# Performance work log

Measured on AMD Instinct MI355X. Metric: run time of the kernel, lower is better.

The kernel has to match this reference:

```python
import jax, jax.numpy as jnp
import numpy as np

LN_EPS = 1e-12
CHEB_K = 3
HIDDEN = 64


def _layernorm(x, w, b):
    m = jnp.mean(x, axis=-1, keepdims=True)
    v = jnp.mean((x - m) ** 2, axis=-1, keepdims=True)
    return (x - m) / jnp.sqrt(v + LN_EPS) * w + b


def _magcn(x, node_emb, time_emb, ln_w, ln_b, W_pool, b_pool):
    # x: [B,N,C]; node_emb: [N,D]; W_pool: [D,K,C,O]; b_pool: [D,O]
    e = _layernorm(node_emb + time_emb[None, :], ln_w, ln_b)  # dropout = identity (eval)
    supports = jax.nn.softmax(e @ e.T, axis=1)                # [N,N]
    N = e.shape[0]
    Ts = [jnp.eye(N, dtype=x.dtype), supports]
    for _ in range(2, CHEB_K):
        Ts.append(2.0 * supports @ Ts[-1] - Ts[-2])
    S = jnp.stack(Ts, axis=0)                                 # [K,N,N]
    weights = jnp.einsum('nd,dkio->nkio', e, W_pool)          # [N,K,C,O]
    bias = e @ b_pool                                         # [N,O]
    x_g = jnp.einsum('knm,bmc->bnkc', S, x)                   # [B,N,K,C]
    return jnp.einsum('bnki,nkio->bno', x_g, weights) + bias  # [B,N,O]


def setup_inputs() -> dict:
    key = jax.random.key(0)
    ks = jax.random.split(key, 10)
    B, N, C, H, D = 64, 1024, 64, HIDDEN, 16
    return {
        'x': jax.random.normal(ks[0], (B, N, C), jnp.float32),
        'norm_dis_matrix': jax.random.uniform(ks[1], (N, N), jnp.float32),
        'state': jax.random.normal(ks[2], (B, N, H), jnp.float32),
        'node_embeddings': jax.random.normal(ks[3], (N, D), jnp.float32),
        'node_flows': jax.random.normal(ks[4], (B, N), jnp.float32),
        'time_embeddings': jax.random.normal(ks[5], (D,), jnp.float32),
        'gate_W': jax.random.normal(ks[6], (D, CHEB_K, C + H, 2 * H), jnp.float32) * 0.1,
        'gate_b': jax.random.normal(ks[7], (D, 2 * H), jnp.float32) * 0.1,
        'gate_ln_w': jnp.ones((D,), jnp.float32),
        'gate_ln_b': jnp.zeros((D,), jnp.float32),
        'update_W': jax.random.normal(ks[8], (D, CHEB_K, C + H, H), jnp.float32) * 0.1,
        'update_b': jax.random.normal(ks[9], (D, H), jnp.float32) * 0.1,
        'update_ln_w': jnp.ones((D,), jnp.float32),
        'update_ln_b': jnp.zeros((D,), jnp.float32),
    }


def reference(x, norm_dis_matrix, state, node_embeddings, node_flows, time_embeddings,
              gate_W, gate_b, gate_ln_w, gate_ln_b,
              update_W, update_b, update_ln_w, update_ln_b):
    inp_state = jnp.concatenate([x, state], axis=-1)  # [B,N,C+H]
    z_r = jax.nn.sigmoid(_magcn(inp_state, node_embeddings, time_embeddings,
                                gate_ln_w, gate_ln_b, gate_W, gate_b))
    z, r = z_r[..., :HIDDEN], z_r[..., HIDDEN:]
    candidate = jnp.concatenate([x, z * state], axis=-1)
    hc = jnp.tanh(_magcn(candidate, node_embeddings, time_embeddings,
                         update_ln_w, update_ln_b, update_W, update_b))
    return r * state + (1.0 - r) * hc
```

## Files before the change

### kernel.cpp

```cpp
#include <hip/hip_runtime.h>
#include <hip/hip_bf16.h>

typedef __hip_bfloat16 bf16;
typedef __attribute__((ext_vector_type(8))) short bf16x8;
typedef __attribute__((ext_vector_type(4))) float f32x4;

constexpr int Bn = 64;
constexpr int Nn = 1024;
constexpr int Dd = 16;
constexpr int Cc = 64;
constexpr int Hh = 64;
constexpr int CI = 128;
constexpr int OG = 128;
constexpr int OU = 64;
constexpr int Jt = Bn * CI;

__device__ __forceinline__ float b2f(bf16 v) { return __bfloat162float(v); }
__device__ __forceinline__ float lo2f(unsigned u) { return __uint_as_float(u << 16); }
__device__ __forceinline__ float hi2f(unsigned u) { return __uint_as_float(u & 0xffff0000u); }
__device__ __forceinline__ float bfbits2f(unsigned short u) { return __uint_as_float(((unsigned)u) << 16); }
__device__ __forceinline__ unsigned short f2bfbits(float x) {
    bf16 h = __float2bfloat16(x);
    return *reinterpret_cast<unsigned short*>(&h);
}

__device__ __forceinline__ float ldin(const void* p, size_t i, int flag) {
    return flag ? b2f(((const bf16*)p)[i]) : ((const float*)p)[i];
}
__device__ __forceinline__ void ld4(const void* p, size_t idx, int f, float* o) {
    if (f) {
        const ushort4 u = *(const ushort4*)((const unsigned short*)p + idx);
        o[0] = bfbits2f(u.x); o[1] = bfbits2f(u.y); o[2] = bfbits2f(u.z); o[3] = bfbits2f(u.w);
    } else {
        const float4 v = *(const float4*)((const float*)p + idx);
        o[0] = v.x; o[1] = v.y; o[2] = v.z; o[3] = v.w;
    }
}

__device__ __forceinline__ void gload_lds16(const void* g, void* l) {
    __builtin_amdgcn_global_load_lds((const __attribute__((address_space(1))) void*)g,
                                     (__attribute__((address_space(3))) void*)l, 16, 0, 0);
}

__global__ void detect_kernel(const void* glnw, int* flag) {
    unsigned u = *(const unsigned*)glnw;
    *flag = (u == 0x3F800000u) ? 0 : 1;
}

__global__ void conv_f32(const void* __restrict__ src, float* __restrict__ dst,
                         int n, const int* __restrict__ flag) {
    const int f = *flag;
    for (int i = blockIdx.x * blockDim.x + threadIdx.x; i < n; i += gridDim.x * blockDim.x)
        dst[i] = ldin(src, i, f);
}
__global__ void conv_bf(const void* __restrict__ src, bf16* __restrict__ dst,
                        int n, const int* __restrict__ flag) {
    const int f = *flag;
    for (int i = blockIdx.x * blockDim.x + threadIdx.x; i < n; i += gridDim.x * blockDim.x)
        dst[i] = f ? ((const bf16*)src)[i] : __float2bfloat16(((const float*)src)[i]);
}

__global__ void ln_kernel(const void* __restrict__ nemb, const void* __restrict__ temb,
                          const void* __restrict__ wg, const void* __restrict__ bg,
                          const void* __restrict__ wu, const void* __restrict__ bu,
                          float* __restrict__ e_g, float* __restrict__ e_u,
                          const int* __restrict__ flag) {
    const int f = *flag;
    int t = blockIdx.x * blockDim.x + threadIdx.x;
    if (t >= 2 * Nn) return;
    int which = t >> 10;
    int n = t & (Nn - 1);
    float v[Dd];
    float mean = 0.f;
#pragma unroll
    for (int d = 0; d < Dd; d++) { v[d] = ldin(nemb, n * Dd + d, f) + ldin(temb, d, f); mean += v[d]; }
    mean *= (1.f / Dd);
    float var = 0.f;
#pragma unroll
    for (int d = 0; d < Dd; d++) { float c = v[d] - mean; var += c * c; }
    var *= (1.f / Dd);
    float inv = 1.f / sqrtf(var + 1e-12f);
    const void* w = which ? wu : wg;
    const void* bb = which ? bu : bg;
    float* e = which ? e_u : e_g;
#pragma unroll
    for (int d = 0; d < Dd; d++)
        e[n * Dd + d] = (v[d] - mean) * inv * ldin(w, d, f) + ldin(bb, d, f);
}

__global__ __launch_bounds__(256) void attn_kernel(const float* __restrict__ e, bf16* __restrict__ A) {
    __shared__ float en[Dd];
    __shared__ float logits[Nn];
    __shared__ float red[256];
    const int n = blockIdx.x, t = threadIdx.x;
    if (t < Dd) en[t] = e[n * Dd + t];
    __syncthreads();
    float lmax = -1e30f;
    for (int m = t; m < Nn; m += 256) {
        float s = 0.f;
#pragma unroll
        for (int d = 0; d < Dd; d++) s += en[d] * e[m * Dd + d];
        logits[m] = s;
        lmax = fmaxf(lmax, s);
    }
    red[t] = lmax; __syncthreads();
    for (int s = 128; s > 0; s >>= 1) { if (t < s) red[t] = fmaxf(red[t], red[t + s]); __syncthreads(); }
    const float M = red[0];
    __syncthreads();
    float lsum = 0.f;
    for (int m = t; m < Nn; m += 256) { float p = expf(logits[m] - M); logits[m] = p; lsum += p; }
    red[t] = lsum; __syncthreads();
    for (int s = 128; s > 0; s >>= 1) { if (t < s) red[t] += red[t + s]; __syncthreads(); }
    const float inv = 1.f / red[0];
    for (int m = t; m < Nn; m += 256) A[(size_t)n * Nn + m] = __float2bfloat16(logits[m] * inv);
}

__global__ __launch_bounds__(256) void build_xg0(const void* __restrict__ x, const void* __restrict__ oth,
                                                 bf16* __restrict__ xg0t,
                                                 const int* __restrict__ flag, int oth_bf16) {
    const int f = *flag;
    const int b = blockIdx.x;
    const int n0 = blockIdx.y * 64;
    __shared__ bf16 tile[128][68];
    const int t = threadIdx.x;
#pragma unroll
    for (int idx = t; idx < 64 * 128; idx += 256) {
        const int n = idx >> 7, i = idx & 127;
        const size_t base = ((size_t)b << 10) + n0 + n;
        float v;
        if (i < Cc) v = ldin(x, base * Cc + i, f);
        else v = oth_bf16 ? b2f(((const bf16*)oth)[base * Hh + i - Cc])
                          : ldin(oth, base * Hh + i - Cc, f);
        tile[i][n] = __float2bfloat16(v);
    }
    __syncthreads();
#pragma unroll
    for (int idx = t; idx < 128 * 64; idx += 256) {
        const int i = idx >> 6, n = idx & 63;
        xg0t[((size_t)(b * CI + i) << 10) + n0 + n] = tile[i][n];
    }
}

__global__ __launch_bounds__(256) void agg_mfma(const bf16* __restrict__ Amat,
                                                const bf16* __restrict__ Xmat,
                                                const bf16* __restrict__ Sub,
                                                bf16* __restrict__ Cmat,
                                                int cheb) {
    __shared__ bf16 Atile[128 * 32];
    __shared__ bf16 Xtile[128 * 32];
    char* AtileC = (char*)Atile;
    char* XtileC = (char*)Xtile;

    const int t = threadIdx.x;
    const int lane = t & 63, w = t >> 6;
    const int j0 = blockIdx.x * 128;
    const int m0 = blockIdx.y * 128;
    const int wr = (w >> 1) * 64, wc = (w & 1) * 64;
    const int lr = lane & 15, lq = lane >> 4;

    f32x4 acc[4][4];
#pragma unroll
    for (int a = 0; a < 4; a++)
#pragma unroll
        for (int b = 0; b < 4; b++) acc[a][b] = (f32x4){0.f, 0.f, 0.f, 0.f};

    const int srow = w * 16 + (lane >> 2);
    const int scb = (lane & 3) * 16;

    for (int k0 = 0; k0 < Nn; k0 += 32) {
        __syncthreads();
#pragma unroll
        for (int p = 0; p < 2; p++) {
            const int row = p * 64 + srow;
            gload_lds16((const char*)Amat + (size_t)(m0 + row) * 2048 + k0 * 2 + scb,
                        AtileC + p * 4096 + w * 1024);
            gload_lds16((const char*)Xmat + (size_t)(j0 + row) * 2048 + k0 * 2 + scb,
                        XtileC + p * 4096 + w * 1024);
        }
        __syncthreads();
        bf16x8 af[4], xf[4];
#pragma unroll
        for (int fr = 0; fr < 4; fr++)
            af[fr] = *(const bf16x8*)(AtileC + (wr + fr * 16 + lr) * 64 + lq * 16);
#pragma unroll
        for (int fc = 0; fc < 4; fc++)
            xf[fc] = *(const bf16x8*)(XtileC + (wc + fc * 16 + lr) * 64 + lq * 16);
#pragma unroll
        for (int fr = 0; fr < 4; fr++)
#pragma unroll
            for (int fc = 0; fc < 4; fc++)
                acc[fr][fc] = __builtin_amdgcn_mfma_f32_16x16x32_bf16(af[fr], xf[fc], acc[fr][fc], 0, 0, 0);
    }

#pragma unroll
    for (int fr = 0; fr < 4; fr++) {
        const int m = m0 + wr + fr * 16 + lq * 4;
#pragma unroll
        for (int fc = 0; fc < 4; fc++) {
            const int j = j0 + wc + fc * 16 + lr;
            f32x4 v = acc[fr][fc];
            const size_t off = ((size_t)j << 10) + m;
            if (cheb) {
                const ushort4 s = *(const ushort4*)((const unsigned short*)Sub + off);
                v.x = 2.f * v.x - bfbits2f(s.x);
                v.y = 2.f * v.y - bfbits2f(s.y);
                v.z = 2.f * v.z - bfbits2f(s.z);
                v.w = 2.f * v.w - bfbits2f(s.w);
            }
            ushort4 o;
            o.x = f2bfbits(v.x); o.y = f2bfbits(v.y); o.z = f2bfbits(v.z); o.w = f2bfbits(v.w);
            *(ushort4*)((unsigned short*)Cmat + off) = o;
        }
    }
}

__global__ __launch_bounds__(256) void t2s_kernel(const bf16* __restrict__ src1, bf16* __restrict__ dst1,
                                                  const bf16* __restrict__ src2, bf16* __restrict__ dst2) {
    const bf16* src = blockIdx.z ? src2 : src1;
    bf16* dst = blockIdx.z ? dst2 : dst1;
    const int b = blockIdx.x;
    const int n0 = blockIdx.y * 64;
    __shared__ bf16 tile[128][68];
    const int t = threadIdx.x;
#pragma unroll
    for (int idx = t; idx < 128 * 64; idx += 256) {
        const int i = idx >> 6, n = idx & 63;
        tile[i][n] = src[((size_t)(b * CI + i) << 10) + n0 + n];
    }
    __syncthreads();
#pragma unroll
    for (int idx = t; idx < 64 * 128; idx += 256) {
        const int n = idx >> 7, i = idx & 127;
        dst[(((size_t)b << 10) + n0 + n) * CI + i] = tile[i][n];
    }
}

__global__ __launch_bounds__(256) void gate_gemm(const void* __restrict__ x, const void* __restrict__ state,
                                                 const bf16* __restrict__ xg1, const bf16* __restrict__ xg2,
                                                 const float* __restrict__ e,
                                                 const unsigned short* __restrict__ Wb,
                                                 const float* __restrict__ bpool,
                                                 bf16* __restrict__ zs, float* __restrict__ r_s,
                                                 const int* __restrict__ flag) {
    const int f = *flag;
    const int n = blockIdx.x, t = threadIdx.x;
    __shared__ float en[Dd];
    __shared__ float bias[OG];
    __shared__ float Xs[64][17];
    __shared__ float Ws[16][OG];
    if (t < Dd) en[t] = e[n * Dd + t];
    __syncthreads();
    if (t < OG) {
        float s = 0.f;
#pragma unroll
        for (int d = 0; d < Dd; d++) s += en[d] * bpool[d * OG + t];
        bias[t] = s;
    }
    const int ty = t >> 4, tx = t & 15;
    float acc[4][8] = {};
    for (int kt = 0; kt < 24; kt++) {
        const int ch = kt >> 3;
        const int i0 = (kt & 7) * 16;
        __syncthreads();
        {
            const int b_ = t >> 2, i4 = (t & 3) * 4;
            const int ii = i0 + i4;
            const size_t base = ((size_t)b_ << 10) + n;
            float v[4];
            if (ch == 0) {
                if (ii < Cc) ld4(x, base * Cc + ii, f, v);
                else ld4(state, base * Hh + (ii - Cc), f, v);
            } else {
                const bf16* s = (ch == 1) ? xg1 : xg2;
                const ushort4 u = *(const ushort4*)((const unsigned short*)s + base * CI + ii);
                v[0] = bfbits2f(u.x); v[1] = bfbits2f(u.y); v[2] = bfbits2f(u.z); v[3] = bfbits2f(u.w);
            }
            Xs[b_][i4 + 0] = v[0]; Xs[b_][i4 + 1] = v[1]; Xs[b_][i4 + 2] = v[2]; Xs[b_][i4 + 3] = v[3];
        }
        {
            const int i = t >> 4, o0 = (t & 15) * 8;
            float wacc[8] = {};
            const unsigned short* wp = Wb + ((size_t)ch * CI + (i0 + i)) * OG + o0;
#pragma unroll
            for (int d = 0; d < Dd; d++) {
                const uint4 u = *(const uint4*)(wp + (size_t)d * (3 * CI * OG));
                const float ed = en[d];
                wacc[0] += ed * lo2f(u.x); wacc[1] += ed * hi2f(u.x);
                wacc[2] += ed * lo2f(u.y); wacc[3] += ed * hi2f(u.y);
                wacc[4] += ed * lo2f(u.z); wacc[5] += ed * hi2f(u.z);
                wacc[6] += ed * lo2f(u.w); wacc[7] += ed * hi2f(u.w);
            }
#pragma unroll
            for (int j = 0; j < 8; j++) Ws[i][o0 + j] = wacc[j];
        }
        __syncthreads();
#pragma unroll
        for (int kk = 0; kk < 16; kk++) {
            float a[4], bv[8];
#pragma unroll
            for (int i = 0; i < 4; i++) a[i] = Xs[ty * 4 + i][kk];
#pragma unroll
            for (int j = 0; j < 8; j++) bv[j] = Ws[kk][tx + 16 * j];
#pragma unroll
            for (int i = 0; i < 4; i++)
#pragma unroll
                for (int j = 0; j < 8; j++) acc[i][j] += a[i] * bv[j];
        }
    }
#pragma unroll
    for (int i = 0; i < 4; i++) {
        const int b_ = ty * 4 + i;
        const size_t base = ((size_t)b_ << 10) + n;
#pragma unroll
        for (int j = 0; j < 8; j++) {
            const int o = tx + 16 * j;
            const float v = acc[i][j] + bias[o];
            const float sg = 1.f / (1.f + expf(-v));
            if (o < Hh) {
                const float st = ldin(state, base * Hh + o, f);
                zs[base * Hh + o] = __float2bfloat16(sg * st);
            } else {
                r_s[base * Hh + (o - Hh)] = sg;
            }
        }
    }
}

__global__ __launch_bounds__(256) void upd_gemm(const void* __restrict__ x, const bf16* __restrict__ zs,
                                                const bf16* __restrict__ xg1, const bf16* __restrict__ xg2,
                                                const float* __restrict__ e,
                                                const unsigned short* __restrict__ Wb,
                                                const float* __restrict__ bpool,
                                                const float* __restrict__ r_s,
                                                const void* __restrict__ state,
                                                void* __restrict__ out,
                                                const int* __restrict__ flag) {
    const int f = *flag;
    const int n = blockIdx.x, t = threadIdx.x;
    __shared__ float en[Dd];
    __shared__ float bias[OU];
    __shared__ float Xs[64][17];
    __shared__ float Ws[16][OU];
    if (t < Dd) en[t] = e[n * Dd + t];
    __syncthreads();
    if (t < OU) {
        float s = 0.f;
#pragma unroll
        for (int d = 0; d < Dd; d++) s += en[d] * bpool[d * OU + t];
        bias[t] = s;
    }
    const int ty = t >> 4, tx = t & 15;
    float acc[4][4] = {};
    for (int kt = 0; kt < 24; kt++) {
        const int ch = kt >> 3;
        const int i0 = (kt & 7) * 16;
        __syncthreads();
        {
            const int b_ = t >> 2, i4 = (t & 3) * 4;
            const int ii = i0 + i4;
            const size_t base = ((size_t)b_ << 10) + n;
            float v[4];
            if (ch == 0) {
                if (ii < Cc) ld4(x, base * Cc + ii, f, v);
                else {
                    const ushort4 u = *(const ushort4*)((const unsigned short*)zs + base * Hh + (ii - Cc));
                    v[0] = bfbits2f(u.x); v[1] = bfbits2f(u.y); v[2] = bfbits2f(u.z); v[3] = bfbits2f(u.w);
                }
            } else {
                const bf16* s = (ch == 1) ? xg1 : xg2;
                const ushort4 u = *(const ushort4*)((const unsigned short*)s + base * CI + ii);
                v[0] = bfbits2f(u.x); v[1] = bfbits2f(u.y); v[2] = bfbits2f(u.z); v[3] = bfbits2f(u.w);
            }
            Xs[b_][i4 + 0] = v[0]; Xs[b_][i4 + 1] = v[1]; Xs[b_][i4 + 2] = v[2]; Xs[b_][i4 + 3] = v[3];
        }
        {
            const int i = t >> 4, o0 = (t & 15) * 4;
            float wacc[4] = {};
            const unsigned short* wp = Wb + ((size_t)ch * CI + (i0 + i)) * OU + o0;
#pragma unroll
            for (int d = 0; d < Dd; d++) {
                const uint2 u = *(const uint2*)(wp + (size_t)d * (3 * CI * OU));
                const float ed = en[d];
                wacc[0] += ed * lo2f(u.x); wacc[1] += ed * hi2f(u.x);
                wacc[2] += ed * lo2f(u.y); wacc[3] += ed * hi2f(u.y);
            }
#pragma unroll
            for (int j = 0; j < 4; j++) Ws[i][o0 + j] = wacc[j];
        }
        __syncthreads();
#pragma unroll
        for (int kk = 0; kk < 16; kk++) {
            float a[4], bv[4];
#pragma unroll
            for (int i = 0; i < 4; i++) a[i] = Xs[ty * 4 + i][kk];
#pragma unroll
            for (int j = 0; j < 4; j++) bv[j] = Ws[kk][tx + 16 * j];
#pragma unroll
            for (int i = 0; i < 4; i++)
#pragma unroll
                for (int j = 0; j < 4; j++) acc[i][j] += a[i] * bv[j];
        }
    }
#pragma unroll
    for (int i = 0; i < 4; i++) {
        const int b_ = ty * 4 + i;
        const size_t base = ((size_t)b_ << 10) + n;
#pragma unroll
        for (int j = 0; j < 4; j++) {
            const int o = tx + 16 * j;
            const float hc = tanhf(acc[i][j] + bias[o]);
            const size_t idx = base * Hh + o;
            const float r = r_s[idx];
            const float st = ldin(state, idx, f);
            const float v = r * st + (1.f - r) * hc;
            if (f) ((bf16*)out)[idx] = __float2bfloat16(v);
            else   ((float*)out)[idx] = v;
        }
    }
}

extern "C" void kernel_launch(void* const* d_in, const int* in_sizes, int n_in,
                              void* d_out, int out_size, void* d_ws, size_t ws_size,
                              hipStream_t stream) {
    const void* x     = d_in[0];
    const void* state = d_in[2];
    const void* nemb  = d_in[3];
    const void* temb  = d_in[5];
    const void* gW    = d_in[6];
    const void* gb    = d_in[7];
    const void* glnw  = d_in[8];
    const void* glnb  = d_in[9];
    const void* uW    = d_in[10];
    const void* ub    = d_in[11];
    const void* ulnw  = d_in[12];
    const void* ulnb  = d_in[13];

    constexpr int GW_N = Dd * 3 * CI * OG;
    constexpr int GB_N = Dd * OG;
    constexpr int UW_N = Dd * 3 * CI * OU;
    constexpr int UB_N = Dd * OU;

    char* base = (char*)d_ws;
    size_t off = 0;
    auto carve = [&](size_t bytes) { char* p = base + off; off += (bytes + 255) & ~(size_t)255; return p; };
    int*   flag = (int*)carve(4);
    unsigned short* gWb = (unsigned short*)carve(GW_N * 2);
    unsigned short* uWb = (unsigned short*)carve(UW_N * 2);
    float* gbf = (float*)carve(GB_N * 4);
    float* ubf = (float*)carve(UB_N * 4);
    float* e_g = (float*)carve(Nn * Dd * 4);
    float* e_u = (float*)carve(Nn * Dd * 4);
    bf16*  Abf = (bf16*)carve((size_t)Nn * Nn * 2);
    bf16*  xg0t = (bf16*)carve((size_t)Jt * Nn * 2);
    bf16*  xg1t = (bf16*)carve((size_t)Jt * Nn * 2);
    bf16*  xg2t = (bf16*)carve((size_t)Jt * Nn * 2);
    bf16*  xg1s = (bf16*)carve((size_t)Jt * Nn * 2);
    bf16*  xg2s = (bf16*)carve((size_t)Jt * Nn * 2);
    bf16*  zs  = (bf16*)carve((size_t)Bn * Nn * Hh * 2);
    float* r_s = (float*)carve((size_t)Bn * Nn * Hh * 4);
    if (ws_size < off) return;

    detect_kernel<<<1, 1, 0, stream>>>(glnw, flag);
    conv_bf<<<(GW_N + 255) / 256, 256, 0, stream>>>(gW, (bf16*)gWb, GW_N, flag);
    conv_bf<<<(UW_N + 255) / 256, 256, 0, stream>>>(uW, (bf16*)uWb, UW_N, flag);
    conv_f32<<<(GB_N + 255) / 256, 256, 0, stream>>>(gb, gbf, GB_N, flag);
    conv_f32<<<(UB_N + 255) / 256, 256, 0, stream>>>(ub, ubf, UB_N, flag);
    ln_kernel<<<8, 256, 0, stream>>>(nemb, temb, glnw, glnb, ulnw, ulnb, e_g, e_u, flag);

    attn_kernel<<<Nn, 256, 0, stream>>>(e_g, Abf);
    build_xg0<<<dim3(Bn, 16), 256, 0, stream>>>(x, state, xg0t, flag, 0);
    agg_mfma<<<dim3(Jt / 128, Nn / 128), 256, 0, stream>>>(Abf, xg0t, nullptr, xg1t, 0);
    agg_mfma<<<dim3(Jt / 128, Nn / 128), 256, 0, stream>>>(Abf, xg1t, xg0t, xg2t, 1);
    t2s_kernel<<<dim3(Bn, 16, 2), 256, 0, stream>>>(xg1t, xg1s, xg2t, xg2s);
    gate_gemm<<<Nn, 256, 0, stream>>>(x, state, xg1s, xg2s, e_g, gWb, gbf, zs, r_s, flag);

    attn_kernel<<<Nn, 256, 0, stream>>>(e_u, Abf);
    build_xg0<<<dim3(Bn, 16), 256, 0, stream>>>(x, zs, xg0t, flag, 1);
    agg_mfma<<<dim3(Jt / 128, Nn / 128), 256, 0, stream>>>(Abf, xg0t, nullptr, xg1t, 0);
    agg_mfma<<<dim3(Jt / 128, Nn / 128), 256, 0, stream>>>(Abf, xg1t, xg0t, xg2t, 1);
    t2s_kernel<<<dim3(Bn, 16, 2), 256, 0, stream>>>(xg1t, xg1s, xg2t, xg2s);
    upd_gemm<<<Nn, 256, 0, stream>>>(x, zs, xg1s, xg2s, e_u, uWb, ubf, r_s, state, d_out, flag);
}
```

Before: 565.0 us.

## Replace per-node FMA GEMMs with MFMA kernel and fuse transposes into aggregation

```diff
diff --git a/kernel.cpp b/kernel.cpp
--- a/kernel.cpp
+++ b/kernel.cpp
@@ -26,15 +26,6 @@
 
 __device__ __forceinline__ float ldin(const void* p, size_t i, int flag) {
     return flag ? b2f(((const bf16*)p)[i]) : ((const float*)p)[i];
-}
-__device__ __forceinline__ void ld4(const void* p, size_t idx, int f, float* o) {
-    if (f) {
-        const ushort4 u = *(const ushort4*)((const unsigned short*)p + idx);
-        o[0] = bfbits2f(u.x); o[1] = bfbits2f(u.y); o[2] = bfbits2f(u.z); o[3] = bfbits2f(u.w);
-    } else {
-        const float4 v = *(const float4*)((const float*)p + idx);
-        o[0] = v.x; o[1] = v.y; o[2] = v.z; o[3] = v.w;
-    }
 }
 
 __device__ __forceinline__ void gload_lds16(const void* g, void* l) {
@@ -116,7 +107,7 @@
 }
 
 __global__ __launch_bounds__(256) void build_xg0(const void* __restrict__ x, const void* __restrict__ oth,
-                                                 bf16* __restrict__ xg0t,
+                                                 bf16* __restrict__ xg0t, bf16* __restrict__ xg0s,
                                                  const int* __restrict__ flag, int oth_bf16) {
     const int f = *flag;
     const int b = blockIdx.x;
@@ -132,6 +123,7 @@
         else v = oth_bf16 ? b2f(((const bf16*)oth)[base * Hh + i - Cc])
                           : ldin(oth, base * Hh + i - Cc, f);
         tile[i][n] = __float2bfloat16(v);
+        xg0s[base * CI + i] = tile[i][n];
     }
     __syncthreads();
 #pragma unroll
@@ -144,8 +136,9 @@
 __global__ __launch_bounds__(256) void agg_mfma(const bf16* __restrict__ Amat,
                                                 const bf16* __restrict__ Xmat,
                                                 const bf16* __restrict__ Sub,
-                                                bf16* __restrict__ Cmat,
-                                                int cheb) {
+                                                bf16* __restrict__ Ct,
+                                                bf16* __restrict__ Cs,
+                                                int cheb, int write_t) {
     __shared__ bf16 Atile[128 * 32];
     __shared__ bf16 Xtile[128 * 32];
     char* AtileC = (char*)Atile;
@@ -207,214 +200,171 @@
                 v.z = 2.f * v.z - bfbits2f(s.z);
                 v.w = 2.f * v.w - bfbits2f(s.w);
             }
-            ushort4 o;
-            o.x = f2bfbits(v.x); o.y = f2bfbits(v.y); o.z = f2bfbits(v.z); o.w = f2bfbits(v.w);
-            *(ushort4*)((unsigned short*)Cmat + off) = o;
-        }
-    }
-}
-
-__global__ __launch_bounds__(256) void t2s_kernel(const bf16* __restrict__ src1, bf16* __restrict__ dst1,
-                                                  const bf16* __restrict__ src2, bf16* __restrict__ dst2) {
-    const bf16* src = blockIdx.z ? src2 : src1;
-    bf16* dst = blockIdx.z ? dst2 : dst1;
-    const int b = blockIdx.x;
-    const int n0 = blockIdx.y * 64;
-    __shared__ bf16 tile[128][68];
+            ushort4 o4;
+            o4.x = f2bfbits(v.x); o4.y = f2bfbits(v.y); o4.z = f2bfbits(v.z); o4.w = f2bfbits(v.w);
+            if (write_t) *(ushort4*)((unsigned short*)Ct + off) = o4;
+            const int b = j >> 7, i = j & 127;
+            unsigned short* ps = (unsigned short*)Cs;
+            const unsigned short* pv = (const unsigned short*)&o4;
+#pragma unroll
+            for (int q = 0; q < 4; q++)
+                ps[((((size_t)b << 10) + m + q) << 7) + i] = pv[q];
+        }
+    }
+}
+
+constexpr int WROWB = 272;
+
+__global__ __launch_bounds__(256, 2) void pernode_gemm(
+    const bf16* __restrict__ x0, const bf16* __restrict__ x1, const bf16* __restrict__ x2,
+    const float* __restrict__ e, const unsigned short* __restrict__ Wb,
+    const float* __restrict__ bpool,
+    const void* __restrict__ state, const float* __restrict__ r_in,
+    bf16* __restrict__ zs, float* __restrict__ r_out, void* __restrict__ out,
+    const int* __restrict__ flag, int OSTR, int two_per_node, int is_upd)
+{
+    const int f = *flag;
+    const int bx = blockIdx.x;
+    const int n = two_per_node ? (bx >> 1) : bx;
+    const int obase = two_per_node ? ((bx & 1) << 6) : 0;
+
+    __shared__ bf16 Xc[64 * 128];
+    __shared__ bf16 Whi[64 * (WROWB / 2)];
+    __shared__ bf16 Wlo[64 * (WROWB / 2)];
+    __shared__ float enS[16];
+    __shared__ float biasS[64];
+    char* XcC = (char*)Xc;
+    char* WhiC = (char*)Whi;
+    char* WloC = (char*)Wlo;
+
     const int t = threadIdx.x;
-#pragma unroll
-    for (int idx = t; idx < 128 * 64; idx += 256) {
-        const int i = idx >> 6, n = idx & 63;
-        tile[i][n] = src[((size_t)(b * CI + i) << 10) + n0 + n];
-    }
+    const int lane = t & 63, w = t >> 6;
+    const int lr = lane & 15, lq = lane >> 4;
+
+    if (t < 16) enS[t] = e[n * 16 + t];
     __syncthreads();
-#pragma unroll
-    for (int idx = t; idx < 64 * 128; idx += 256) {
-        const int n = idx >> 7, i = idx & 127;
-        dst[(((size_t)b << 10) + n0 + n) * CI + i] = tile[i][n];
-    }
-}
-
-__global__ __launch_bounds__(256) void gate_gemm(const void* __restrict__ x, const void* __restrict__ state,
-                                                 const bf16* __restrict__ xg1, const bf16* __restrict__ xg2,
-                                                 const float* __restrict__ e,
-                                                 const unsigned short* __restrict__ Wb,
-                                                 const float* __restrict__ bpool,
-                                                 bf16* __restrict__ zs, float* __restrict__ r_s,
-                                                 const int* __restrict__ flag) {
-    const int f = *flag;
-    const int n = blockIdx.x, t = threadIdx.x;
-    __shared__ float en[Dd];
-    __shared__ float bias[OG];
-    __shared__ float Xs[64][17];
-    __shared__ float Ws[16][OG];
-    if (t < Dd) en[t] = e[n * Dd + t];
-    __syncthreads();
-    if (t < OG) {
+    if (t < 64) {
         float s = 0.f;
 #pragma unroll
-        for (int d = 0; d < Dd; d++) s += en[d] * bpool[d * OG + t];
-        bias[t] = s;
-    }
-    const int ty = t >> 4, tx = t & 15;
-    float acc[4][8] = {};
-    for (int kt = 0; kt < 24; kt++) {
-        const int ch = kt >> 3;
-        const int i0 = (kt & 7) * 16;
+        for (int d = 0; d < 16; d++) s += enS[d] * bpool[d * OSTR + obase + t];
+        biasS[t] = s;
+    }
+    float enr[16];
+#pragma unroll
+    for (int d = 0; d < 16; d++) enr[d] = enS[d];
+
+    const int krow0 = (t >> 4) * 8;
+    const int ocol = (t & 15) * 4;
+
+    f32x4 acc[4];
+#pragma unroll
+    for (int i = 0; i < 4; i++) acc[i] = (f32x4){0.f, 0.f, 0.f, 0.f};
+
+    const bf16* xs[3] = {x0, x1, x2};
+
+    for (int ch = 0; ch < 3; ch++) {
         __syncthreads();
         {
-            const int b_ = t >> 2, i4 = (t & 3) * 4;
-            const int ii = i0 + i4;
-            const size_t base = ((size_t)b_ << 10) + n;
-            float v[4];
-            if (ch == 0) {
-                if (ii < Cc) ld4(x, base * Cc + ii, f, v);
-                else ld4(state, base * Hh + (ii - Cc), f, v);
+            const bf16* Xsrc = xs[ch];
+#pragma unroll
+            for (int p = 0; p < 4; p++) {
+                const int row = p * 16 + w * 4 + (lane >> 4);
+                const int colg = (lane & 15) ^ (row & 7);
+                gload_lds16(Xsrc + (((size_t)row << 10) + n) * 128 + colg * 8,
+                            XcC + (p * 16 + w * 4) * 256);
+            }
+        }
+        float wacc[8][4];
+#pragma unroll
+        for (int r = 0; r < 8; r++)
+#pragma unroll
+            for (int c = 0; c < 4; c++) wacc[r][c] = 0.f;
+        {
+            const unsigned short* wp0 = Wb + (size_t)(ch * 128 + krow0) * OSTR + obase + ocol;
+#pragma unroll 2
+            for (int d = 0; d < 16; d++) {
+                const unsigned short* wp = wp0 + (size_t)d * 384 * OSTR;
+                const float ed = enr[d];
+#pragma unroll
+                for (int r = 0; r < 8; r++) {
+                    const uint2 u = *(const uint2*)(wp + r * OSTR);
+                    wacc[r][0] += ed * lo2f(u.x);
+                    wacc[r][1] += ed * hi2f(u.x);
+                    wacc[r][2] += ed * lo2f(u.y);
+                    wacc[r][3] += ed * hi2f(u.y);
+                }
+            }
+        }
+        __syncthreads();
+#pragma unroll
+        for (int c = 0; c < 4; c++) {
+            unsigned short hbuf[8], lbuf[8];
+#pragma unroll
+            for (int r = 0; r < 8; r++) {
+                const float v = wacc[r][c];
+                const unsigned short h = f2bfbits(v);
+                hbuf[r] = h;
+                lbuf[r] = f2bfbits(v - bfbits2f(h));
+            }
+            uint4 hv, lv;
+            hv.x = hbuf[0] | ((unsigned)hbuf[1] << 16);
+            hv.y = hbuf[2] | ((unsigned)hbuf[3] << 16);
+            hv.z = hbuf[4] | ((unsigned)hbuf[5] << 16);
+            hv.w = hbuf[6] | ((unsigned)hbuf[7] << 16);
+            lv.x = lbuf[0] | ((unsigned)lbuf[1] << 16);
+            lv.y = lbuf[2] | ((unsigned)lbuf[3] << 16);
+            lv.z = lbuf[4] | ((unsigned)lbuf[5] << 16);
+            lv.w = lbuf[6] | ((unsigned)lbuf[7] << 16);
+            *(uint4*)(WhiC + (ocol + c) * WROWB + krow0 * 2) = hv;
+            *(uint4*)(WloC + (ocol + c) * WROWB + krow0 * 2) = lv;
+        }
+        __syncthreads();
+#pragma unroll
+        for (int ks = 0; ks < 4; ks++) {
+            bf16x8 af;
+            {
+                const int row = w * 16 + lr;
+                const int col16 = (ks * 4 + lq) ^ (row & 7);
+                af = *(const bf16x8*)(XcC + row * 256 + col16 * 16);
+            }
+#pragma unroll
+            for (int fc = 0; fc < 4; fc++) {
+                const bf16x8 bh = *(const bf16x8*)(WhiC + (fc * 16 + lr) * WROWB + ks * 64 + lq * 16);
+                acc[fc] = __builtin_amdgcn_mfma_f32_16x16x32_bf16(af, bh, acc[fc], 0, 0, 0);
+            }
+#pragma unroll
+            for (int fc = 0; fc < 4; fc++) {
+                const bf16x8 bl = *(const bf16x8*)(WloC + (fc * 16 + lr) * WROWB + ks * 64 + lq * 16);
+                acc[fc] = __builtin_amdgcn_mfma_f32_16x16x32_bf16(af, bl, acc[fc], 0, 0, 0);
+            }
+        }
+    }
+
+#pragma unroll
+    for (int fc = 0; fc < 4; fc++) {
+        const int ol = fc * 16 + lr;
+        const float bias = biasS[ol];
+#pragma unroll
+        for (int q = 0; q < 4; q++) {
+            const int b = w * 16 + lq * 4 + q;
+            const size_t idx = (((size_t)b << 10) + n) * 64 + ol;
+            const float v = acc[fc][q] + bias;
+            if (is_upd) {
+                const float hc = tanhf(v);
+                const float r = r_in[idx];
+                const float st = ldin(state, idx, f);
+                const float o = r * st + (1.f - r) * hc;
+                if (f) ((bf16*)out)[idx] = __float2bfloat16(o);
+                else   ((float*)out)[idx] = o;
             } else {
-                const bf16* s = (ch == 1) ? xg1 : xg2;
-                const ushort4 u = *(const ushort4*)((const unsigned short*)s + base * CI + ii);
-                v[0] = bfbits2f(u.x); v[1] = bfbits2f(u.y); v[2] = bfbits2f(u.z); v[3] = bfbits2f(u.w);
-            }
-            Xs[b_][i4 + 0] = v[0]; Xs[b_][i4 + 1] = v[1]; Xs[b_][i4 + 2] = v[2]; Xs[b_][i4 + 3] = v[3];
-        }
-        {
-            const int i = t >> 4, o0 = (t & 15) * 8;
-            float wacc[8] = {};
-            const unsigned short* wp = Wb + ((size_t)ch * CI + (i0 + i)) * OG + o0;
-#pragma unroll
-            for (int d = 0; d < Dd; d++) {
-                const uint4 u = *(const uint4*)(wp + (size_t)d * (3 * CI * OG));
-                const float ed = en[d];
-                wacc[0] += ed * lo2f(u.x); wacc[1] += ed * hi2f(u.x);
-                wacc[2] += ed * lo2f(u.y); wacc[3] += ed * hi2f(u.y);
-                wacc[4] += ed * lo2f(u.z); wacc[5] += ed * hi2f(u.z);
-                wacc[6] += ed * lo2f(u.w); wacc[7] += ed * hi2f(u.w);
-            }
-#pragma unroll
-            for (int j = 0; j < 8; j++) Ws[i][o0 + j] = wacc[j];
-        }
-        __syncthreads();
-#pragma unroll
-        for (int kk = 0; kk < 16; kk++) {
-            float a[4], bv[8];
-#pragma unroll
-            for (int i = 0; i < 4; i++) a[i] = Xs[ty * 4 + i][kk];
-#pragma unroll
-            for (int j = 0; j < 8; j++) bv[j] = Ws[kk][tx + 16 * j];
-#pragma unroll
-            for (int i = 0; i < 4; i++)
-#pragma unroll
-                for (int j = 0; j < 8; j++) acc[i][j] += a[i] * bv[j];
-        }
-    }
-#pragma unroll
-    for (int i = 0; i < 4; i++) {
-        const int b_ = ty * 4 + i;
-        const size_t base = ((size_t)b_ << 10) + n;
-#pragma unroll
-        for (int j = 0; j < 8; j++) {
-            const int o = tx + 16 * j;
-            const float v = acc[i][j] + bias[o];
-            const float sg = 1.f / (1.f + expf(-v));
-            if (o < Hh) {
-                const float st = ldin(state, base * Hh + o, f);
-                zs[base * Hh + o] = __float2bfloat16(sg * st);
-            } else {
-                r_s[base * Hh + (o - Hh)] = sg;
-            }
-        }
-    }
-}
-
-__global__ __launch_bounds__(256) void upd_gemm(const void* __restrict__ x, const bf16* __restrict__ zs,
-                                                const bf16* __restrict__ xg1, const bf16* __restrict__ xg2,
-                                                const float* __restrict__ e,
-                                                const unsigned short* __restrict__ Wb,
-                                                const float* __restrict__ bpool,
-                                                const float* __restrict__ r_s,
-                                                const void* __restrict__ state,
-                                                void* __restrict__ out,
-                                                const int* __restrict__ flag) {
-    const int f = *flag;
-    const int n = blockIdx.x, t = threadIdx.x;
-    __shared__ float en[Dd];
-    __shared__ float bias[OU];
-    __shared__ float Xs[64][17];
-    __shared__ float Ws[16][OU];
-    if (t < Dd) en[t] = e[n * Dd + t];
-    __syncthreads();
-    if (t < OU) {
-        float s = 0.f;
-#pragma unroll
-        for (int d = 0; d < Dd; d++) s += en[d] * bpool[d * OU + t];
-        bias[t] = s;
-    }
-    const int ty = t >> 4, tx = t & 15;
-    float acc[4][4] = {};
-    for (int kt = 0; kt < 24; kt++) {
-        const int ch = kt >> 3;
-        const int i0 = (kt & 7) * 16;
-        __syncthreads();
-        {
-            const int b_ = t >> 2, i4 = (t & 3) * 4;
-            const int ii = i0 + i4;
-            const size_t base = ((size_t)b_ << 10) + n;
-            float v[4];
-            if (ch == 0) {
-                if (ii < Cc) ld4(x, base * Cc + ii, f, v);
-                else {
-                    const ushort4 u = *(const ushort4*)((const unsigned short*)zs + base * Hh + (ii - Cc));
-                    v[0] = bfbits2f(u.x); v[1] = bfbits2f(u.y); v[2] = bfbits2f(u.z); v[3] = bfbits2f(u.w);
+                const float sg = 1.f / (1.f + expf(-v));
+                if (obase == 0) {
+                    const float st = ldin(state, idx, f);
+                    zs[idx] = __float2bfloat16(sg * st);
+                } else {
+                    r_out[idx] = sg;
                 }
-            } else {
-                const bf16* s = (ch == 1) ? xg1 : xg2;
-                const ushort4 u = *(const ushort4*)((const unsigned short*)s + base * CI + ii);
-                v[0] = bfbits2f(u.x); v[1] = bfbits2f(u.y); v[2] = bfbits2f(u.z); v[3] = bfbits2f(u.w);
-            }
-            Xs[b_][i4 + 0] = v[0]; Xs[b_][i4 + 1] = v[1]; Xs[b_][i4 + 2] = v[2]; Xs[b_][i4 + 3] = v[3];
-        }
-        {
-            const int i = t >> 4, o0 = (t & 15) * 4;
-            float wacc[4] = {};
-            const unsigned short* wp = Wb + ((size_t)ch * CI + (i0 + i)) * OU + o0;
-#pragma unroll
-            for (int d = 0; d < Dd; d++) {
-                const uint2 u = *(const uint2*)(wp + (size_t)d * (3 * CI * OU));
-                const float ed = en[d];
-                wacc[0] += ed * lo2f(u.x); wacc[1] += ed * hi2f(u.x);
-                wacc[2] += ed * lo2f(u.y); wacc[3] += ed * hi2f(u.y);
-            }
-#pragma unroll
-            for (int j = 0; j < 4; j++) Ws[i][o0 + j] = wacc[j];
-        }
-        __syncthreads();
-#pragma unroll
-        for (int kk = 0; kk < 16; kk++) {
-            float a[4], bv[4];
-#pragma unroll
-            for (int i = 0; i < 4; i++) a[i] = Xs[ty * 4 + i][kk];
-#pragma unroll
-            for (int j = 0; j < 4; j++) bv[j] = Ws[kk][tx + 16 * j];
-#pragma unroll
-            for (int i = 0; i < 4; i++)
-#pragma unroll
-                for (int j = 0; j < 4; j++) acc[i][j] += a[i] * bv[j];
-        }
-    }
-#pragma unroll
-    for (int i = 0; i < 4; i++) {
-        const int b_ = ty * 4 + i;
-        const size_t base = ((size_t)b_ << 10) + n;
-#pragma unroll
-        for (int j = 0; j < 4; j++) {
-            const int o = tx + 16 * j;
-            const float hc = tanhf(acc[i][j] + bias[o]);
-            const size_t idx = base * Hh + o;
-            const float r = r_s[idx];
-            const float st = ldin(state, idx, f);
-            const float v = r * st + (1.f - r) * hc;
-            if (f) ((bf16*)out)[idx] = __float2bfloat16(v);
-            else   ((float*)out)[idx] = v;
+            }
         }
     }
 }
@@ -450,14 +400,14 @@
     float* ubf = (float*)carve(UB_N * 4);
     float* e_g = (float*)carve(Nn * Dd * 4);
     float* e_u = (float*)carve(Nn * Dd * 4);
-    bf16*  Abf = (bf16*)carve((size_t)Nn * Nn * 2);
+    bf16*  Abf  = (bf16*)carve((size_t)Nn * Nn * 2);
     bf16*  xg0t = (bf16*)carve((size_t)Jt * Nn * 2);
+    bf16*  xg0s = (bf16*)carve((size_t)Jt * Nn * 2);
     bf16*  xg1t = (bf16*)carve((size_t)Jt * Nn * 2);
-    bf16*  xg2t = (bf16*)carve((size_t)Jt * Nn * 2);
     bf16*  xg1s = (bf16*)carve((size_t)Jt * Nn * 2);
     bf16*  xg2s = (bf16*)carve((size_t)Jt * Nn * 2);
-    bf16*  zs  = (bf16*)carve((size_t)Bn * Nn * Hh * 2);
-    float* r_s = (float*)carve((size_t)Bn * Nn * Hh * 4);
+    bf16*  zs   = (bf16*)carve((size_t)Bn * Nn * Hh * 2);
+    float* r_s  = (float*)carve((size_t)Bn * Nn * Hh * 4);
     if (ws_size < off) return;
 
     detect_kernel<<<1, 1, 0, stream>>>(glnw, flag);
@@ -468,16 +418,16 @@
     ln_kernel<<<8, 256, 0, stream>>>(nemb, temb, glnw, glnb, ulnw, ulnb, e_g, e_u, flag);
 
     attn_kernel<<<Nn, 256, 0, stream>>>(e_g, Abf);
-    build_xg0<<<dim3(Bn, 16), 256, 0, stream>>>(x, state, xg0t, flag, 0);
-    agg_mfma<<<dim3(Jt / 128, Nn / 128), 256, 0, stream>>>(Abf, xg0t, nullptr, xg1t, 0);
-    agg_mfma<<<dim3(Jt / 128, Nn / 128), 256, 0, stream>>>(Abf, xg1t, xg0t, xg2t, 1);
-    t2s_kernel<<<dim3(Bn, 16, 2), 256, 0, stream>>>(xg1t, xg1s, xg2t, xg2s);
-    gate_gemm<<<Nn, 256, 0, stream>>>(x, state, xg1s, xg2s, e_g, gWb, gbf, zs, r_s, flag);
+    build_xg0<<<dim3(Bn, 16), 256, 0, stream>>>(x, state, xg0t, xg0s, flag, 0);
+    agg_mfma<<<dim3(Jt / 128, Nn / 128), 256, 0, stream>>>(Abf, xg0t, nullptr, xg1t, xg1s, 0, 1);
+    agg_mfma<<<dim3(Jt / 128, Nn / 128), 256, 0, stream>>>(Abf, xg1t, xg0t, xg1t, xg2s, 1, 0);
+    pernode_gemm<<<2 * Nn, 256, 0, stream>>>(xg0s, xg1s, xg2s, e_g, gWb, gbf,
+                                             state, nullptr, zs, r_s, nullptr, flag, OG, 1, 0);
 
     attn_kernel<<<Nn, 256, 0, stream>>>(e_u, Abf);
-    build_xg0<<<dim3(Bn, 16), 256, 0, stream>>>(x, zs, xg0t, flag, 1);
-    agg_mfma<<<dim3(Jt / 128, Nn / 128), 256, 0, stream>>>(Abf, xg0t, nullptr, xg1t, 0);
-    agg_mfma<<<dim3(Jt / 128, Nn / 128), 256, 0, stream>>>(Abf, xg1t, xg0t, xg2t, 1);
-    t2s_kernel<<<dim3(Bn, 16, 2), 256, 0, stream>>>(xg1t, xg1s, xg2t, xg2s);
-    upd_gemm<<<Nn, 256, 0, stream>>>(x, zs, xg1s, xg2s, e_u, uWb, ubf, r_s, state, d_out, flag);
-}
+    build_xg0<<<dim3(Bn, 16), 256, 0, stream>>>(x, zs, xg0t, xg0s, flag, 1);
+    agg_mfma<<<dim3(Jt / 128, Nn / 128), 256, 0, stream>>>(Abf, xg0t, nullptr, xg1t, xg1s, 0, 1);
+    agg_mfma<<<dim3(Jt / 128, Nn / 128), 256, 0, stream>>>(Abf, xg1t, xg0t, xg1t, xg2s, 1, 0);
+    pernode_gemm<<<Nn, 256, 0, stream>>>(xg0s, xg1s, xg2s, e_u, uWb, ubf,
+                                         state, r_s, nullptr, nullptr, d_out, flag, OU, 0, 1);
+}
```

Measured after the change: 486.1 us. -14.0%, faster.
